# Kernel tuning notes

Measured on AMD Instinct MI355X. Metric: run time of the kernel, lower is better.

The kernel has to match this reference:

```python
import jax, jax.numpy as jnp
import numpy as np

N, E, D_IN, D_E, D_OUT = 100000, 1250000, 64, 64, 64


def setup_inputs() -> dict:
    key = jax.random.key(0)
    ks = jax.random.split(key, 8)
    return {
        "nfeats": jax.random.normal(ks[0], (N, 1, D_IN), dtype=jnp.float32),
        "efeats": jax.random.normal(ks[1], (E, 1, D_E), dtype=jnp.float32),
        "src": jax.random.randint(ks[2], (E,), 0, N, dtype=jnp.int32),
        "dst": jax.random.randint(ks[3], (E,), 0, N, dtype=jnp.int32),
        "W_msg": jax.random.normal(ks[4], (D_OUT, D_IN + D_E), dtype=jnp.float32) * 0.08,
        "b_msg": jax.random.normal(ks[5], (D_OUT,), dtype=jnp.float32) * 0.02,
        "W_apply": jax.random.normal(ks[6], (D_OUT, D_IN + D_OUT), dtype=jnp.float32) * 0.08,
        "b_apply": jax.random.normal(ks[7], (D_OUT,), dtype=jnp.float32) * 0.02,
    }


def reference(nfeats, efeats, src, dst, W_msg, b_msg, W_apply, b_apply):
    n = nfeats.shape[0]
    # per-edge message: Linear(cat(src_h, edge_h))  -> [E, 1, D_OUT]
    edge_in = jnp.concatenate([nfeats[src], efeats], axis=-1)  # [E,1,D_IN+D_E]
    m = jnp.einsum('ekd,od->eko', edge_in, W_msg) + b_msg
    # mean segment-reduce over destination nodes (empty segments -> 0, like DGL mean)
    msum = jax.ops.segment_sum(m, dst, num_segments=n)  # [N,1,D_OUT]
    cnt = jax.ops.segment_sum(jnp.ones((dst.shape[0],), dtype=m.dtype), dst, num_segments=n)
    h_neigh = msum / jnp.maximum(cnt, 1.0)[:, None, None]
    # apply: relu(Linear(cat(h, h_neigh)))
    node_in = jnp.concatenate([nfeats, h_neigh], axis=-1)  # [N,1,D_IN+D_OUT]
    return jax.nn.relu(jnp.einsum('nkd,od->nko', node_in, W_apply) + b_apply)
```

## Files before the change

### kernel.cpp

```cpp
#include <hip/hip_runtime.h>
#include <hip/hip_bf16.h>


typedef __attribute__((ext_vector_type(8))) short bf16x8;
typedef __attribute__((ext_vector_type(4))) short bf16x4;
typedef __attribute__((ext_vector_type(4))) float f32x4;
typedef __attribute__((ext_vector_type(2))) int i32x2;

__device__ __forceinline__ short f2bf(float f) {
  union { float f; unsigned u; } v; v.f = f;
  unsigned u = v.u;
  u += 0x7fffu + ((u >> 16) & 1u);
  return (short)(u >> 16);
}

__device__ __forceinline__ bf16x8 pack8(float4 a, float4 b) {
  bf16x8 r;
  r[0] = f2bf(a.x); r[1] = f2bf(a.y); r[2] = f2bf(a.z); r[3] = f2bf(a.w);
  r[4] = f2bf(b.x); r[5] = f2bf(b.y); r[6] = f2bf(b.z); r[7] = f2bf(b.w);
  return r;
}

__device__ __forceinline__ bf16x4 pack4(f32x4 a) {
  bf16x4 r;
  r[0] = f2bf(a[0]); r[1] = f2bf(a[1]); r[2] = f2bf(a[2]); r[3] = f2bf(a[3]);
  return r;
}

__global__ __launch_bounds__(256) void prep_hist_k(
    const float* __restrict__ nf, const float* __restrict__ Wm,
    const float* __restrict__ Wa, short* __restrict__ nf16,
    short* __restrict__ wpack, const int* __restrict__ dst,
    int* __restrict__ hist, int conv_blocks, long total_nf, int E, int hist_blocks)
{
  const int bx = blockIdx.x;
  if (bx < conv_blocks) {
    long t = (long)bx * 256 + threadIdx.x;
    long b8 = t * 8;
    if (b8 + 8 <= total_nf) {
      const float* p = nf + b8;
      *(bf16x8*)(nf16 + b8) = pack8(*(const float4*)p, *(const float4*)(p + 4));
    }
  } else if (bx == conv_blocks) {
    int t = threadIdx.x;
#pragma unroll
    for (int j = 0; j < 8; ++j) {
      int id = t * 8 + j;
      int w = id >> 10, kc = (id >> 8) & 3, nc = (id >> 6) & 3, lane = id & 63;
      int r = lane & 15, g = lane >> 4;
      const float* W = w ? Wa : Wm;
      const float* p = W + (nc * 16 + r) * 128 + kc * 32 + g * 8;
      *(bf16x8*)(wpack + (long)id * 8) = pack8(*(const float4*)p, *(const float4*)(p + 4));
    }
  } else {
    const int hb = bx - conv_blocks - 1;
    int i4 = hb * 256 + threadIdx.x;
    const int stride = hist_blocks * 256;
    const int E4 = E >> 2;
    for (; i4 < E4; i4 += stride) {
      const int4 d = ((const int4*)dst)[i4];
      atomicAdd(&hist[d.x], 1);
      atomicAdd(&hist[d.y], 1);
      atomicAdd(&hist[d.z], 1);
      atomicAdd(&hist[d.w], 1);
    }
    if (hb == 0) {
      int i = (E & ~3) + (int)threadIdx.x;
      if (i < E) atomicAdd(&hist[dst[i]], 1);
    }
  }
}

__global__ __launch_bounds__(256) void scan1_k(const int* __restrict__ hist,
                                               int* __restrict__ off,
                                               int* __restrict__ parts, int N) {
  __shared__ int sh[256];
  int tid = threadIdx.x;
  int base = blockIdx.x * 1024 + tid * 4;
  int v[4], ts = 0;
#pragma unroll
  for (int j = 0; j < 4; ++j) {
    int idx = base + j;
    v[j] = (idx < N) ? hist[idx] : 0;
    ts += v[j];
  }
  sh[tid] = ts;
  __syncthreads();
  for (int o = 1; o < 256; o <<= 1) {
    int y = (tid >= o) ? sh[tid - o] : 0;
    __syncthreads();
    sh[tid] += y;
    __syncthreads();
  }
  int run = sh[tid] - ts;
#pragma unroll
  for (int j = 0; j < 4; ++j) {
    int idx = base + j;
    if (idx < N) off[idx] = run;
    run += v[j];
  }
  if (tid == 255) parts[blockIdx.x] = sh[255];
}

__global__ void scan2_k(int* __restrict__ parts, int* __restrict__ off,
                        int nparts, int N, int E) {
  int lane = threadIdx.x & 63;
  int i0 = 2 * lane, i1 = 2 * lane + 1;
  int p0 = (i0 < nparts) ? parts[i0] : 0;
  int p1 = (i1 < nparts) ? parts[i1] : 0;
  int s = p0 + p1;
  int x = s;
  for (int o = 1; o < 64; o <<= 1) {
    int y = __shfl_up(x, o);
    if (lane >= o) x += y;
  }
  int ex = x - s;
  if (i0 < nparts) parts[i0] = ex;
  if (i1 < nparts) parts[i1] = ex + p0;
  if (lane == 0) off[N] = E;
}

__global__ __launch_bounds__(256) void scan3_k(int* __restrict__ off,
                                               int* __restrict__ woff,
                                               const int* __restrict__ parts, int N) {
  int p = parts[blockIdx.x];
  int base = blockIdx.x * 1024 + threadIdx.x;
#pragma unroll
  for (int j = 0; j < 4; ++j) {
    int idx = base + j * 256;
    if (idx < N) {
      int v = off[idx] + p;
      off[idx] = v;
      woff[idx] = v;
    }
  }
}

__global__ __launch_bounds__(256) void bin_k(
    const int* __restrict__ src, const int* __restrict__ dst,
    int* __restrict__ woff, i32x2* __restrict__ packed, int E) {
  int i4 = blockIdx.x * blockDim.x + threadIdx.x;
  const int stride = gridDim.x * blockDim.x;
  const int E4 = E >> 2;
  for (; i4 < E4; i4 += stride) {
    const int4 d = ((const int4*)dst)[i4];
    const int4 s = ((const int4*)src)[i4];
    const int e0 = i4 * 4;
    int p;
    i32x2 v;
    p = atomicAdd(&woff[d.x], 1); v[0] = e0 + 0; v[1] = s.x;
    __builtin_nontemporal_store(v, &packed[p]);
    p = atomicAdd(&woff[d.y], 1); v[0] = e0 + 1; v[1] = s.y;
    __builtin_nontemporal_store(v, &packed[p]);
    p = atomicAdd(&woff[d.z], 1); v[0] = e0 + 2; v[1] = s.z;
    __builtin_nontemporal_store(v, &packed[p]);
    p = atomicAdd(&woff[d.w], 1); v[0] = e0 + 3; v[1] = s.w;
    __builtin_nontemporal_store(v, &packed[p]);
  }
  if (blockIdx.x == 0) {
    int i = (E & ~3) + (int)threadIdx.x;
    if (i < E) {
      int p = atomicAdd(&woff[dst[i]], 1);
      i32x2 v; v[0] = i; v[1] = src[i];
      __builtin_nontemporal_store(v, &packed[p]);
    }
  }
}

__global__ __launch_bounds__(256) void reduce_k(
    const float* __restrict__ nf, const float* __restrict__ ef,
    const int* __restrict__ off, const i32x2* __restrict__ packed,
    short* __restrict__ ssum16, int N)
{
  const int wave = (blockIdx.x * blockDim.x + threadIdx.x) >> 6;
  const int lane = threadIdx.x & 63;
  if (wave >= N) return;
  const int g = lane >> 4;
  const int s = lane & 15;
  const int beg = off[wave], end = off[wave + 1];

  f32x4 anf = {0.f, 0.f, 0.f, 0.f};
  f32x4 aef = {0.f, 0.f, 0.f, 0.f};

  int i = beg;
  for (; i + 8 <= end; i += 8) {
    const i32x2 p0 = __builtin_nontemporal_load(&packed[i + g]);
    const i32x2 p1 = __builtin_nontemporal_load(&packed[i + 4 + g]);
    const f32x4 x0 = *(const f32x4*)(nf + (size_t)p0[1] * 64 + s * 4);
    const f32x4 y0 = __builtin_nontemporal_load((const f32x4*)(ef + (size_t)p0[0] * 64 + s * 4));
    const f32x4 x1 = *(const f32x4*)(nf + (size_t)p1[1] * 64 + s * 4);
    const f32x4 y1 = __builtin_nontemporal_load((const f32x4*)(ef + (size_t)p1[0] * 64 + s * 4));
    anf += x0 + x1;
    aef += y0 + y1;
  }
  if (i + 4 <= end) {
    const i32x2 p0 = __builtin_nontemporal_load(&packed[i + g]);
    const f32x4 x0 = *(const f32x4*)(nf + (size_t)p0[1] * 64 + s * 4);
    const f32x4 y0 = __builtin_nontemporal_load((const f32x4*)(ef + (size_t)p0[0] * 64 + s * 4));
    anf += x0;
    aef += y0;
    i += 4;
  }
  if (g < end - i) {
    const i32x2 p0 = __builtin_nontemporal_load(&packed[i + g]);
    const f32x4 x0 = *(const f32x4*)(nf + (size_t)p0[1] * 64 + s * 4);
    const f32x4 y0 = __builtin_nontemporal_load((const f32x4*)(ef + (size_t)p0[0] * 64 + s * 4));
    anf += x0;
    aef += y0;
  }

#pragma unroll
  for (int m = 16; m <= 32; m <<= 1) {
#pragma unroll
    for (int c = 0; c < 4; ++c) {
      anf[c] += __shfl_xor(anf[c], m);
      aef[c] += __shfl_xor(aef[c], m);
    }
  }

  short* row = ssum16 + (size_t)wave * 128;
  if (g == 0) {
    __builtin_nontemporal_store(pack4(anf), (bf16x4*)(row + s * 4));
  } else if (g == 1) {
    __builtin_nontemporal_store(pack4(aef), (bf16x4*)(row + 64 + s * 4));
  }
}

__global__ __launch_bounds__(256) void node_apply(
    const short* __restrict__ nf16, const short* __restrict__ ssum16,
    const int* __restrict__ off, const short* __restrict__ wpack,
    const float* __restrict__ b_msg, const float* __restrict__ b_apply,
    float* __restrict__ out, int ntiles)
{
  __shared__ float hn[4][16 * 68];
  const int wid = threadIdx.x >> 6;
  const int lane = threadIdx.x & 63;
  const int r = lane & 15;
  const int g = lane >> 4;
  const int tile = blockIdx.x * 4 + wid;
  if (tile >= ntiles) return;
  const int n0 = tile * 16;

  bf16x8 wm[4][4], wa[4][4];
#pragma unroll
  for (int kc = 0; kc < 4; ++kc)
#pragma unroll
    for (int nc = 0; nc < 4; ++nc) {
      wm[kc][nc] = *(const bf16x8*)(wpack + ((long)((0 * 4 + kc) * 4 + nc) * 64 + lane) * 8);
      wa[kc][nc] = *(const bf16x8*)(wpack + ((long)((1 * 4 + kc) * 4 + nc) * 64 + lane) * 8);
    }

  f32x4 acc[4] = {};
#pragma unroll
  for (int kc = 0; kc < 4; ++kc) {
    const bf16x8 af = *(const bf16x8*)(ssum16 + (size_t)(n0 + r) * 128 + kc * 32 + g * 8);
#pragma unroll
    for (int nc = 0; nc < 4; ++nc)
      acc[nc] = __builtin_amdgcn_mfma_f32_16x16x32_bf16(af, wm[kc][nc], acc[nc], 0, 0, 0);
  }

  float cn[4];
#pragma unroll
  for (int q = 0; q < 4; ++q) {
    int n = n0 + g * 4 + q;
    cn[q] = (float)(off[n + 1] - off[n]);
  }
#pragma unroll
  for (int nc = 0; nc < 4; ++nc) {
    const float bm = b_msg[nc * 16 + r];
#pragma unroll
    for (int q = 0; q < 4; ++q) {
      const float v = cn[q] > 0.f ? acc[nc][q] / cn[q] + bm : 0.f;
      hn[wid][(g * 4 + q) * 68 + nc * 16 + r] = v;
    }
  }

  f32x4 acc2[4] = {};
#pragma unroll
  for (int kc = 0; kc < 2; ++kc) {
    const bf16x8 af = *(const bf16x8*)(nf16 + (size_t)(n0 + r) * 64 + kc * 32 + g * 8);
#pragma unroll
    for (int nc = 0; nc < 4; ++nc)
      acc2[nc] = __builtin_amdgcn_mfma_f32_16x16x32_bf16(af, wa[kc][nc], acc2[nc], 0, 0, 0);
  }
#pragma unroll
  for (int kc = 2; kc < 4; ++kc) {
    const float* p = &hn[wid][r * 68 + (kc - 2) * 32 + g * 8];
    const bf16x8 af = pack8(*(const float4*)p, *(const float4*)(p + 4));
#pragma unroll
    for (int nc = 0; nc < 4; ++nc)
      acc2[nc] = __builtin_amdgcn_mfma_f32_16x16x32_bf16(af, wa[kc][nc], acc2[nc], 0, 0, 0);
  }

#pragma unroll
  for (int nc = 0; nc < 4; ++nc) {
    const float ba = b_apply[nc * 16 + r];
#pragma unroll
    for (int q = 0; q < 4; ++q) {
      float v = acc2[nc][q] + ba;
      v = v > 0.f ? v : 0.f;
      __builtin_nontemporal_store(v, &out[(size_t)(n0 + g * 4 + q) * 64 + nc * 16 + r]);
    }
  }
}

extern "C" void kernel_launch(void* const* d_in, const int* in_sizes, int n_in,
                              void* d_out, int out_size, void* d_ws, size_t ws_size,
                              hipStream_t stream) {
  const float* nfeats  = (const float*)d_in[0];
  const float* efeats  = (const float*)d_in[1];
  const int*   src     = (const int*)d_in[2];
  const int*   dst     = (const int*)d_in[3];
  const float* W_msg   = (const float*)d_in[4];
  const float* b_msg   = (const float*)d_in[5];
  const float* W_apply = (const float*)d_in[6];
  const float* b_apply = (const float*)d_in[7];
  float* out = (float*)d_out;

  const int N = in_sizes[0] / 64;
  const int E = in_sizes[2];
  const int nparts = (N + 1023) / 1024;

  auto alignup = [](size_t x) { return (x + 127) & ~(size_t)127; };
  char* ws = (char*)d_ws;
  size_t o = 0;
  int*  hist   = (int*)(ws + o);  o = alignup(o + (size_t)N * 4);
  int*  off    = (int*)(ws + o);  o = alignup(o + (size_t)(N + 1) * 4);
  int*  woff   = (int*)(ws + o);  o = alignup(o + (size_t)N * 4);
  int*  parts  = (int*)(ws + o);  o = alignup(o + (size_t)nparts * 4);
  i32x2* packed = (i32x2*)(ws + o); o = alignup(o + (size_t)E * 8);
  short* ssum16 = (short*)(ws + o); o = alignup(o + (size_t)N * 128 * 2);
  short* nf16   = (short*)(ws + o); o = alignup(o + (size_t)N * 64 * 2);
  short* wpack  = (short*)(ws + o); o = alignup(o + (size_t)2048 * 8 * 2);

  hipMemsetAsync(hist, 0, (size_t)N * 4, stream);

  const long total_nf = (long)N * 64;
  const int conv_blocks = (int)((total_nf / 8 + 255) / 256);
  const int hist_blocks = 1024;
  prep_hist_k<<<conv_blocks + 1 + hist_blocks, 256, 0, stream>>>(
      nfeats, W_msg, W_apply, nf16, wpack, dst, hist,
      conv_blocks, total_nf, E, hist_blocks);
  scan1_k<<<nparts, 256, 0, stream>>>(hist, off, parts, N);
  scan2_k<<<1, 64, 0, stream>>>(parts, off, nparts, N, E);
  scan3_k<<<nparts, 256, 0, stream>>>(off, woff, parts, N);
  bin_k<<<1024, 256, 0, stream>>>(src, dst, woff, packed, E);
  reduce_k<<<(N + 3) / 4, 256, 0, stream>>>(nfeats, efeats, off, packed, ssum16, N);

  const int ntiles = (N + 15) / 16;
  node_apply<<<(ntiles + 3) / 4, 256, 0, stream>>>(nf16, ssum16, off, wpack,
                                                   b_msg, b_apply, out, ntiles);
}
```

Baseline: 650.6 us.

## Fuse CSR build into one cooperative kernel and drop bf16 nfeats pre-conversion

Replaces the memset, histogram, three scan kernels and binning kernel with a single cooperative-launch kernel that uses grid-wide syncs between phases, with the old multi-kernel path kept as a fallback if the cooperative launch fails. It also removes the separate fp32-to-bf16 conversion of node features: node_apply now reads the fp32 features and packs them inline. The goal is to cut launch overhead and an extra pass over the node features. The cost is grid.sync barriers, a scan restricted to 1024 blocks with per-thread serial loops, and heavier fp32 loads in node_apply.

Measured after the change: 1.010 ms. 55.2% more time.

```diff
diff --git a/kernel.cpp b/kernel.cpp
--- a/kernel.cpp
+++ b/kernel.cpp
@@ -1,5 +1,8 @@
 #include <hip/hip_runtime.h>
 #include <hip/hip_bf16.h>
+#include <hip/hip_cooperative_groups.h>
+
+namespace cg = cooperative_groups;
 
 
 typedef __attribute__((ext_vector_type(8))) short bf16x8;
@@ -27,47 +30,148 @@
   return r;
 }
 
-__global__ __launch_bounds__(256) void prep_hist_k(
-    const float* __restrict__ nf, const float* __restrict__ Wm,
-    const float* __restrict__ Wa, short* __restrict__ nf16,
+__device__ __forceinline__ void pack_w_block(const float* __restrict__ Wm,
+                                             const float* __restrict__ Wa,
+                                             short* __restrict__ wpack, int tid) {
+#pragma unroll
+  for (int j = 0; j < 8; ++j) {
+    int id = tid * 8 + j;
+    int w = id >> 10, kc = (id >> 8) & 3, nc = (id >> 6) & 3, lane = id & 63;
+    int r = lane & 15, g = lane >> 4;
+    const float* W = w ? Wa : Wm;
+    const float* p = W + (nc * 16 + r) * 128 + kc * 32 + g * 8;
+    *(bf16x8*)(wpack + (long)id * 8) = pack8(*(const float4*)p, *(const float4*)(p + 4));
+  }
+}
+
+__global__ __launch_bounds__(256, 8) void csr_k(
+    const float* __restrict__ Wm, const float* __restrict__ Wa,
+    short* __restrict__ wpack,
+    const int* __restrict__ src, const int* __restrict__ dst,
+    int* __restrict__ hist, int* __restrict__ off, int* __restrict__ woff,
+    int* __restrict__ parts, i32x2* __restrict__ packed, int N, int E)
+{
+  cg::grid_group grid = cg::this_grid();
+  const int tid = (int)threadIdx.x;
+  const int bx = (int)blockIdx.x;
+  const int nb = (int)gridDim.x;
+  const int gsz = nb * 256;
+  const int gid = bx * 256 + tid;
+
+  for (int i = gid; i < N; i += gsz) hist[i] = 0;
+  if (bx == 0) pack_w_block(Wm, Wa, wpack, tid);
+  grid.sync();
+
+  {
+    const int E4 = E >> 2;
+    for (int i4 = gid; i4 < E4; i4 += gsz) {
+      const int4 d = ((const int4*)dst)[i4];
+      atomicAdd(&hist[d.x], 1); atomicAdd(&hist[d.y], 1);
+      atomicAdd(&hist[d.z], 1); atomicAdd(&hist[d.w], 1);
+    }
+    if (bx == 0) {
+      int i = (E & ~3) + tid;
+      if (i < E) atomicAdd(&hist[dst[i]], 1);
+    }
+  }
+  grid.sync();
+
+  const int per = (N + nb - 1) / nb;
+  const int cbeg = bx * per;
+  const int cend = min(cbeg + per, N);
+  __shared__ int sred[256];
+  {
+    int s = 0;
+    for (int i = cbeg + tid; i < cend; i += 256) s += hist[i];
+    sred[tid] = s;
+    __syncthreads();
+    for (int o = 128; o > 0; o >>= 1) {
+      if (tid < o) sred[tid] += sred[tid + o];
+      __syncthreads();
+    }
+    if (tid == 0) parts[bx] = sred[0];
+  }
+  grid.sync();
+
+  __shared__ int sh[2048];
+  __shared__ int blkpref;
+  __shared__ int sscan[256];
+  for (int i = tid; i < nb; i += 256) sh[i] = parts[i];
+  __syncthreads();
+  if (tid < 64) {
+    int s = 0;
+    for (int i = tid; i < bx; i += 64) s += sh[i];
+#pragma unroll
+    for (int m = 1; m < 64; m <<= 1) s += __shfl_xor(s, m);
+    if (tid == 0) blkpref = s;
+  }
+  __syncthreads();
+  {
+    const int tper = (per + 255) / 256;
+    const int tbeg = cbeg + tid * tper;
+    const int tend = min(tbeg + tper, cend);
+    int s = 0;
+    for (int i = tbeg; i < tend; ++i) s += hist[i];
+    sscan[tid] = s;
+    __syncthreads();
+    for (int o = 1; o < 256; o <<= 1) {
+      int y = (tid >= o) ? sscan[tid - o] : 0;
+      __syncthreads();
+      sscan[tid] += y;
+      __syncthreads();
+    }
+    int run = blkpref + sscan[tid] - s;
+    for (int i = tbeg; i < tend; ++i) {
+      int h = hist[i];
+      off[i] = run; woff[i] = run;
+      run += h;
+    }
+  }
+  if (bx == 0 && tid == 0) off[N] = E;
+  grid.sync();
+
+  {
+    const int E4 = E >> 2;
+    for (int i4 = gid; i4 < E4; i4 += gsz) {
+      const int4 d = ((const int4*)dst)[i4];
+      const int4 sv = ((const int4*)src)[i4];
+      const int e0 = i4 * 4;
+      int p; i32x2 v;
+      p = atomicAdd(&woff[d.x], 1); v[0] = e0 + 0; v[1] = sv.x; __builtin_nontemporal_store(v, &packed[p]);
+      p = atomicAdd(&woff[d.y], 1); v[0] = e0 + 1; v[1] = sv.y; __builtin_nontemporal_store(v, &packed[p]);
+      p = atomicAdd(&woff[d.z], 1); v[0] = e0 + 2; v[1] = sv.z; __builtin_nontemporal_store(v, &packed[p]);
+      p = atomicAdd(&woff[d.w], 1); v[0] = e0 + 3; v[1] = sv.w; __builtin_nontemporal_store(v, &packed[p]);
+    }
+    if (bx == 0) {
+      int i = (E & ~3) + tid;
+      if (i < E) {
+        int p = atomicAdd(&woff[dst[i]], 1);
+        i32x2 v; v[0] = i; v[1] = src[i];
+        __builtin_nontemporal_store(v, &packed[p]);
+      }
+    }
+  }
+}
+
+__global__ __launch_bounds__(256) void fb_histw_k(
+    const float* __restrict__ Wm, const float* __restrict__ Wa,
     short* __restrict__ wpack, const int* __restrict__ dst,
-    int* __restrict__ hist, int conv_blocks, long total_nf, int E, int hist_blocks)
+    int* __restrict__ hist, int E, int hist_blocks)
 {
-  const int bx = blockIdx.x;
-  if (bx < conv_blocks) {
-    long t = (long)bx * 256 + threadIdx.x;
-    long b8 = t * 8;
-    if (b8 + 8 <= total_nf) {
-      const float* p = nf + b8;
-      *(bf16x8*)(nf16 + b8) = pack8(*(const float4*)p, *(const float4*)(p + 4));
-    }
-  } else if (bx == conv_blocks) {
-    int t = threadIdx.x;
-#pragma unroll
-    for (int j = 0; j < 8; ++j) {
-      int id = t * 8 + j;
-      int w = id >> 10, kc = (id >> 8) & 3, nc = (id >> 6) & 3, lane = id & 63;
-      int r = lane & 15, g = lane >> 4;
-      const float* W = w ? Wa : Wm;
-      const float* p = W + (nc * 16 + r) * 128 + kc * 32 + g * 8;
-      *(bf16x8*)(wpack + (long)id * 8) = pack8(*(const float4*)p, *(const float4*)(p + 4));
-    }
-  } else {
-    const int hb = bx - conv_blocks - 1;
-    int i4 = hb * 256 + threadIdx.x;
-    const int stride = hist_blocks * 256;
-    const int E4 = E >> 2;
-    for (; i4 < E4; i4 += stride) {
-      const int4 d = ((const int4*)dst)[i4];
-      atomicAdd(&hist[d.x], 1);
-      atomicAdd(&hist[d.y], 1);
-      atomicAdd(&hist[d.z], 1);
-      atomicAdd(&hist[d.w], 1);
-    }
-    if (hb == 0) {
-      int i = (E & ~3) + (int)threadIdx.x;
-      if (i < E) atomicAdd(&hist[dst[i]], 1);
-    }
+  const int bx = (int)blockIdx.x;
+  if (bx == 0) { pack_w_block(Wm, Wa, wpack, threadIdx.x); return; }
+  const int hb = bx - 1;
+  int i4 = hb * 256 + threadIdx.x;
+  const int stride = hist_blocks * 256;
+  const int E4 = E >> 2;
+  for (; i4 < E4; i4 += stride) {
+    const int4 d = ((const int4*)dst)[i4];
+    atomicAdd(&hist[d.x], 1); atomicAdd(&hist[d.y], 1);
+    atomicAdd(&hist[d.z], 1); atomicAdd(&hist[d.w], 1);
+  }
+  if (hb == 0) {
+    int i = (E & ~3) + (int)threadIdx.x;
+    if (i < E) atomicAdd(&hist[dst[i]], 1);
   }
 }
 
@@ -146,16 +250,11 @@
     const int4 d = ((const int4*)dst)[i4];
     const int4 s = ((const int4*)src)[i4];
     const int e0 = i4 * 4;
-    int p;
-    i32x2 v;
-    p = atomicAdd(&woff[d.x], 1); v[0] = e0 + 0; v[1] = s.x;
-    __builtin_nontemporal_store(v, &packed[p]);
-    p = atomicAdd(&woff[d.y], 1); v[0] = e0 + 1; v[1] = s.y;
-    __builtin_nontemporal_store(v, &packed[p]);
-    p = atomicAdd(&woff[d.z], 1); v[0] = e0 + 2; v[1] = s.z;
-    __builtin_nontemporal_store(v, &packed[p]);
-    p = atomicAdd(&woff[d.w], 1); v[0] = e0 + 3; v[1] = s.w;
-    __builtin_nontemporal_store(v, &packed[p]);
+    int p; i32x2 v;
+    p = atomicAdd(&woff[d.x], 1); v[0] = e0 + 0; v[1] = s.x; __builtin_nontemporal_store(v, &packed[p]);
+    p = atomicAdd(&woff[d.y], 1); v[0] = e0 + 1; v[1] = s.y; __builtin_nontemporal_store(v, &packed[p]);
+    p = atomicAdd(&woff[d.z], 1); v[0] = e0 + 2; v[1] = s.z; __builtin_nontemporal_store(v, &packed[p]);
+    p = atomicAdd(&woff[d.w], 1); v[0] = e0 + 3; v[1] = s.w; __builtin_nontemporal_store(v, &packed[p]);
   }
   if (blockIdx.x == 0) {
     int i = (E & ~3) + (int)threadIdx.x;
@@ -227,7 +326,7 @@
 }
 
 __global__ __launch_bounds__(256) void node_apply(
-    const short* __restrict__ nf16, const short* __restrict__ ssum16,
+    const float* __restrict__ nf, const short* __restrict__ ssum16,
     const int* __restrict__ off, const short* __restrict__ wpack,
     const float* __restrict__ b_msg, const float* __restrict__ b_apply,
     float* __restrict__ out, int ntiles)
@@ -278,7 +377,8 @@
   f32x4 acc2[4] = {};
 #pragma unroll
   for (int kc = 0; kc < 2; ++kc) {
-    const bf16x8 af = *(const bf16x8*)(nf16 + (size_t)(n0 + r) * 64 + kc * 32 + g * 8);
+    const float* p = nf + (size_t)(n0 + r) * 64 + kc * 32 + g * 8;
+    const bf16x8 af = pack8(*(const float4*)p, *(const float4*)(p + 4));
 #pragma unroll
     for (int nc = 0; nc < 4; ++nc)
       acc2[nc] = __builtin_amdgcn_mfma_f32_16x16x32_bf16(af, wa[kc][nc], acc2[nc], 0, 0, 0);
@@ -317,9 +417,8 @@
   const float* b_apply = (const float*)d_in[7];
   float* out = (float*)d_out;
 
-  const int N = in_sizes[0] / 64;
-  const int E = in_sizes[2];
-  const int nparts = (N + 1023) / 1024;
+  int N = in_sizes[0] / 64;
+  int E = in_sizes[2];
 
   auto alignup = [](size_t x) { return (x + 127) & ~(size_t)127; };
   char* ws = (char*)d_ws;
@@ -327,27 +426,30 @@
   int*  hist   = (int*)(ws + o);  o = alignup(o + (size_t)N * 4);
   int*  off    = (int*)(ws + o);  o = alignup(o + (size_t)(N + 1) * 4);
   int*  woff   = (int*)(ws + o);  o = alignup(o + (size_t)N * 4);
-  int*  parts  = (int*)(ws + o);  o = alignup(o + (size_t)nparts * 4);
+  int*  parts  = (int*)(ws + o);  o = alignup(o + (size_t)2048 * 4);
   i32x2* packed = (i32x2*)(ws + o); o = alignup(o + (size_t)E * 8);
   short* ssum16 = (short*)(ws + o); o = alignup(o + (size_t)N * 128 * 2);
-  short* nf16   = (short*)(ws + o); o = alignup(o + (size_t)N * 64 * 2);
   short* wpack  = (short*)(ws + o); o = alignup(o + (size_t)2048 * 8 * 2);
 
-  hipMemsetAsync(hist, 0, (size_t)N * 4, stream);
-
-  const long total_nf = (long)N * 64;
-  const int conv_blocks = (int)((total_nf / 8 + 255) / 256);
-  const int hist_blocks = 1024;
-  prep_hist_k<<<conv_blocks + 1 + hist_blocks, 256, 0, stream>>>(
-      nfeats, W_msg, W_apply, nf16, wpack, dst, hist,
-      conv_blocks, total_nf, E, hist_blocks);
-  scan1_k<<<nparts, 256, 0, stream>>>(hist, off, parts, N);
-  scan2_k<<<1, 64, 0, stream>>>(parts, off, nparts, N, E);
-  scan3_k<<<nparts, 256, 0, stream>>>(off, woff, parts, N);
-  bin_k<<<1024, 256, 0, stream>>>(src, dst, woff, packed, E);
+  void* cargs[] = {(void*)&W_msg, (void*)&W_apply, (void*)&wpack,
+                   (void*)&src, (void*)&dst, (void*)&hist, (void*)&off,
+                   (void*)&woff, (void*)&parts, (void*)&packed,
+                   (void*)&N, (void*)&E};
+  hipError_t cerr = hipLaunchCooperativeKernel(
+      reinterpret_cast<void*>(csr_k), dim3(1024), dim3(256), cargs, 0, stream);
+  if (cerr != hipSuccess) {
+    const int nparts = (N + 1023) / 1024;
+    hipMemsetAsync(hist, 0, (size_t)N * 4, stream);
+    fb_histw_k<<<1 + 1024, 256, 0, stream>>>(W_msg, W_apply, wpack, dst, hist, E, 1024);
+    scan1_k<<<nparts, 256, 0, stream>>>(hist, off, parts, N);
+    scan2_k<<<1, 64, 0, stream>>>(parts, off, nparts, N, E);
+    scan3_k<<<nparts, 256, 0, stream>>>(off, woff, parts, N);
+    bin_k<<<1024, 256, 0, stream>>>(src, dst, woff, packed, E);
+  }
+
   reduce_k<<<(N + 3) / 4, 256, 0, stream>>>(nfeats, efeats, off, packed, ssum16, N);
 
   const int ntiles = (N + 15) / 16;
-  node_apply<<<(ntiles + 3) / 4, 256, 0, stream>>>(nf16, ssum16, off, wpack,
+  node_apply<<<(ntiles + 3) / 4, 256, 0, stream>>>(nfeats, ssum16, off, wpack,
                                                    b_msg, b_apply, out, ntiles);
 }
```
